# Performance work log

Measured on AMD Instinct MI355X. Metric: run time of the kernel, lower is better.

The kernel has to match this reference:

```python
import jax, jax.numpy as jnp
import numpy as np

NUM_CLASSES = 80
NUM_TOP_QUERIES = 300


def setup_inputs() -> dict:
    key = jax.random.key(0)
    k1, k2, k3 = jax.random.split(key, 3)
    B, Q, C = 256, 1000, NUM_CLASSES
    pred_logits = jax.random.normal(k1, (B, Q, C), dtype=jnp.float32)
    pred_boxes = jax.random.uniform(k2, (B, Q, 4), dtype=jnp.float32)  # cxcywh in [0,1)
    orig_target_sizes = jax.random.uniform(k3, (B, 2), dtype=jnp.float32)  # (W, H) scale
    return {"pred_logits": pred_logits, "pred_boxes": pred_boxes,
            "orig_target_sizes": orig_target_sizes}


def _box_cxcywh_to_xyxy(boxes):
    cx, cy, w, h = jnp.split(boxes, 4, axis=-1)
    return jnp.concatenate([cx - 0.5 * w, cy - 0.5 * h, cx + 0.5 * w, cy + 0.5 * h], axis=-1)


def reference(pred_logits, pred_boxes, orig_target_sizes):
    B, Q, C = pred_logits.shape
    # cxcywh -> xyxy, then scale by [W, H, W, H]
    bbox_pred = _box_cxcywh_to_xyxy(pred_boxes)
    scale = jnp.tile(orig_target_sizes, (1, 2))[:, None, :]  # [B,1,4]
    bbox_pred = bbox_pred * scale
    # focal-loss path: sigmoid + flattened top-k over (Q*C)
    scores_all = jax.nn.sigmoid(pred_logits).reshape(B, Q * C)
    scores, index = jax.lax.top_k(scores_all, NUM_TOP_QUERIES)  # [B,K]
    labels = index % C
    q_index = index // C
    boxes = jnp.take_along_axis(bbox_pred, q_index[:, :, None], axis=1)  # [B,K,4]
    return labels, boxes, scores
```

## Files before the change

kernel.cpp:

```cpp
#include <hip/hip_runtime.h>
#include <hip/hip_bf16.h>

#define BATCH 256
#define NQ 1000
#define NC 80
#define QC 80000
#define KTOP 300
#define NT 1024
#define NBINS 4096
#define CAP 1024
#define T0 2.55f

__device__ __forceinline__ unsigned mono_key(float x) {
    unsigned u = __float_as_uint(x);
    return (u & 0x80000000u) ? ~u : (u | 0x80000000u);
}
__device__ __forceinline__ float inv_key(unsigned k) {
    unsigned u = (k & 0x80000000u) ? (k & 0x7FFFFFFFu) : ~k;
    return __uint_as_float(u);
}

__device__ __forceinline__ float ref_sigmoid(float x) {
    float in = __fmul_rn(0.5f, x);
    float xc = fminf(fmaxf(in, -7.90531110763549805f), 7.90531110763549805f);
    float x2 = __fmul_rn(xc, xc);
    float p = fmaf(x2, -2.76076847742355e-16f, 2.00018790482477e-13f);
    p = fmaf(x2, p, -8.60467152213735e-11f);
    p = fmaf(x2, p,  5.12229709037114e-08f);
    p = fmaf(x2, p,  1.48572235717979e-05f);
    p = fmaf(x2, p,  6.37261928875436e-04f);
    p = fmaf(x2, p,  4.89352455891786e-03f);
    float num = __fmul_rn(xc, p);
    float den = fmaf(x2, 1.19825839466702e-06f, 1.18534705686654e-04f);
    den = fmaf(x2, den, 2.26843463243900e-03f);
    den = fmaf(x2, den, 4.89352518554385e-03f);
    float t = num / den;
    t = (fabsf(in) < 0.0004f) ? in : t;
    return __fadd_rn(0.5f, __fmul_rn(0.5f, t));
}

__global__ __launch_bounds__(NT)
void rtdetr_post_kernel(const float* __restrict__ logits,
                        const float* __restrict__ boxes,
                        const float* __restrict__ sizes,
                        float* __restrict__ out) {
    __shared__ unsigned long long cand[CAP];
    __shared__ unsigned hist[NBINS];
    __shared__ unsigned scan[NT];
    __shared__ unsigned s_tbin, s_count;

    const int b = blockIdx.x;
    const int tid = threadIdx.x;
    const float4* lg4 = (const float4*)(logits + (size_t)b * QC);

    if (tid == 0) s_count = 0;
    __syncthreads();

    for (int i = tid; i < QC / 4; i += NT) {
        float4 v = lg4[i];
        float xs[4] = {v.x, v.y, v.z, v.w};
        #pragma unroll
        for (int j = 0; j < 4; ++j) {
            if (xs[j] >= T0) {
                unsigned pos = atomicAdd(&s_count, 1u);
                if (pos < CAP) {
                    unsigned sk = mono_key(ref_sigmoid(xs[j]));
                    unsigned idx = (unsigned)(i * 4 + j);
                    cand[pos] = ((unsigned long long)sk << 32) | (unsigned)(~idx);
                }
            }
        }
    }
    __syncthreads();
    unsigned cnt = s_count;

    if (cnt < KTOP || cnt > CAP) {
        for (int i = tid; i < NBINS; i += NT) hist[i] = 0;
        if (tid == 0) s_count = 0;
        __syncthreads();
        for (int i = tid; i < QC / 4; i += NT) {
            float4 v = lg4[i];
            atomicAdd(&hist[mono_key(v.x) >> 20], 1u);
            atomicAdd(&hist[mono_key(v.y) >> 20], 1u);
            atomicAdd(&hist[mono_key(v.z) >> 20], 1u);
            atomicAdd(&hist[mono_key(v.w) >> 20], 1u);
        }
        __syncthreads();
        unsigned h0 = hist[tid * 4 + 0], h1 = hist[tid * 4 + 1];
        unsigned h2 = hist[tid * 4 + 2], h3 = hist[tid * 4 + 3];
        scan[tid] = h0 + h1 + h2 + h3;
        __syncthreads();
        for (int off = 1; off < NT; off <<= 1) {
            unsigned v = (tid + off < NT) ? scan[tid + off] : 0u;
            __syncthreads();
            scan[tid] += v;
            __syncthreads();
        }
        unsigned run = (tid + 1 < NT) ? scan[tid + 1] : 0u;
        unsigned hs[4] = {h3, h2, h1, h0};
        #pragma unroll
        for (int j = 0; j < 4; ++j) {
            unsigned bin = (unsigned)(tid * 4 + (3 - j));
            if (run < KTOP && KTOP <= run + hs[j]) s_tbin = bin;
            run += hs[j];
        }
        __syncthreads();
        unsigned thresh = s_tbin << 20;
        thresh = (thresh >= 4096u) ? thresh - 4096u : 0u;
        for (int i = tid; i < QC / 4; i += NT) {
            float4 v = lg4[i];
            float xs[4] = {v.x, v.y, v.z, v.w};
            #pragma unroll
            for (int j = 0; j < 4; ++j) {
                if (mono_key(xs[j]) >= thresh) {
                    unsigned pos = atomicAdd(&s_count, 1u);
                    if (pos < CAP) {
                        unsigned sk = mono_key(ref_sigmoid(xs[j]));
                        unsigned idx = (unsigned)(i * 4 + j);
                        cand[pos] = ((unsigned long long)sk << 32) | (unsigned)(~idx);
                    }
                }
            }
        }
        __syncthreads();
        cnt = s_count; if (cnt > CAP) cnt = CAP;
    }

    if (tid < (int)cnt) {
        unsigned long long my = cand[tid];
        unsigned rank = 0;
        for (unsigned j = 0; j < cnt; ++j) rank += (cand[j] > my) ? 1u : 0u;
        if (rank < KTOP) {
            unsigned sk = (unsigned)(my >> 32);
            unsigned idx = ~((unsigned)my);
            float score = inv_key(sk);
            unsigned label = idx % NC;
            unsigned qi = idx / NC;
            float4 bx = ((const float4*)boxes)[(size_t)b * NQ + qi];
            float W = sizes[b * 2 + 0];
            float H = sizes[b * 2 + 1];
            float x0 = (bx.x - 0.5f * bx.z) * W;
            float y0 = (bx.y - 0.5f * bx.w) * H;
            float x1 = (bx.x + 0.5f * bx.z) * W;
            float y1 = (bx.y + 0.5f * bx.w) * H;
            int o = b * KTOP + (int)rank;
            out[o] = (float)label;
            float* ob = out + BATCH * KTOP;
            ob[(size_t)o * 4 + 0] = x0;
            ob[(size_t)o * 4 + 1] = y0;
            ob[(size_t)o * 4 + 2] = x1;
            ob[(size_t)o * 4 + 3] = y1;
            float* os = out + BATCH * KTOP * 5;
            os[o] = score;
        }
    }
}

extern "C" void kernel_launch(void* const* d_in, const int* in_sizes, int n_in,
                              void* d_out, int out_size, void* d_ws, size_t ws_size,
                              hipStream_t stream) {
    const float* logits = (const float*)d_in[0];
    const float* boxes  = (const float*)d_in[1];
    const float* sizes  = (const float*)d_in[2];
    float* out = (float*)d_out;
    rtdetr_post_kernel<<<BATCH, NT, 0, stream>>>(logits, boxes, sizes, out);
}
```

Baseline: 128.7 us.

## Split threshold scan across multiple blocks per batch with global candidate buffer

Moves the first pass, which filters logits above a fixed threshold, into its own kernel that launches 8 blocks of 256 threads per batch row instead of one 1024-thread block per row. This spreads the memory-bound read over many more workgroups. Candidates are appended to a workspace buffer through global atomics, and a second kernel copies them into shared memory to rank and write the output, running the histogram fallback when needed. The cost is a memset, an extra kernel launch, global atomic contention, and a round trip of the candidate keys through global memory.

```diff
diff --git a/kernel.cpp b/kernel.cpp
--- a/kernel.cpp
+++ b/kernel.cpp
@@ -6,10 +6,14 @@
 #define NC 80
 #define QC 80000
 #define KTOP 300
-#define NT 1024
 #define NBINS 4096
 #define CAP 1024
 #define T0 2.55f
+
+#define SLICES 8
+#define K1_NT 256
+#define F4_PER_SLICE (QC / 4 / SLICES)
+#define K2_NT 1024
 
 __device__ __forceinline__ unsigned mono_key(float x) {
     unsigned u = __float_as_uint(x);
@@ -39,46 +43,59 @@
     return __fadd_rn(0.5f, __fmul_rn(0.5f, t));
 }
 
-__global__ __launch_bounds__(NT)
-void rtdetr_post_kernel(const float* __restrict__ logits,
-                        const float* __restrict__ boxes,
-                        const float* __restrict__ sizes,
-                        float* __restrict__ out) {
-    __shared__ unsigned long long cand[CAP];
-    __shared__ unsigned hist[NBINS];
-    __shared__ unsigned scan[NT];
-    __shared__ unsigned s_tbin, s_count;
+__global__ __launch_bounds__(K1_NT)
+void scan_kernel(const float* __restrict__ logits,
+                 unsigned* __restrict__ counters,
+                 unsigned long long* __restrict__ ckeys) {
+    const int blk = blockIdx.x;
+    const int b = blk / SLICES;
+    const int s = blk % SLICES;
+    const float4* lg4 = (const float4*)(logits + (size_t)b * QC) + s * F4_PER_SLICE;
+    const int base4 = s * F4_PER_SLICE;
 
-    const int b = blockIdx.x;
-    const int tid = threadIdx.x;
-    const float4* lg4 = (const float4*)(logits + (size_t)b * QC);
-
-    if (tid == 0) s_count = 0;
-    __syncthreads();
-
-    for (int i = tid; i < QC / 4; i += NT) {
+    for (int i = threadIdx.x; i < F4_PER_SLICE; i += K1_NT) {
         float4 v = lg4[i];
         float xs[4] = {v.x, v.y, v.z, v.w};
         #pragma unroll
         for (int j = 0; j < 4; ++j) {
             if (xs[j] >= T0) {
-                unsigned pos = atomicAdd(&s_count, 1u);
+                unsigned pos = atomicAdd(&counters[b], 1u);
                 if (pos < CAP) {
                     unsigned sk = mono_key(ref_sigmoid(xs[j]));
-                    unsigned idx = (unsigned)(i * 4 + j);
-                    cand[pos] = ((unsigned long long)sk << 32) | (unsigned)(~idx);
+                    unsigned idx = (unsigned)((base4 + i) * 4 + j);
+                    ckeys[(size_t)b * CAP + pos] =
+                        ((unsigned long long)sk << 32) | (unsigned)(~idx);
                 }
             }
         }
     }
-    __syncthreads();
-    unsigned cnt = s_count;
+}
 
-    if (cnt < KTOP || cnt > CAP) {
-        for (int i = tid; i < NBINS; i += NT) hist[i] = 0;
+__global__ __launch_bounds__(K2_NT)
+void select_kernel(const float* __restrict__ logits,
+                   const float* __restrict__ boxes,
+                   const float* __restrict__ sizes,
+                   const unsigned* __restrict__ counters,
+                   const unsigned long long* __restrict__ ckeys,
+                   float* __restrict__ out) {
+    __shared__ unsigned long long cand[CAP];
+    __shared__ unsigned hist[NBINS];
+    __shared__ unsigned scan[K2_NT];
+    __shared__ unsigned s_tbin, s_count;
+
+    const int b = blockIdx.x;
+    const int tid = threadIdx.x;
+    unsigned cnt = counters[b];
+
+    if (cnt >= KTOP && cnt <= CAP) {
+        if (tid < (int)cnt) cand[tid] = ckeys[(size_t)b * CAP + tid];
+        __syncthreads();
+    } else {
+        const float4* lg4 = (const float4*)(logits + (size_t)b * QC);
+        for (int i = tid; i < NBINS; i += K2_NT) hist[i] = 0;
         if (tid == 0) s_count = 0;
         __syncthreads();
-        for (int i = tid; i < QC / 4; i += NT) {
+        for (int i = tid; i < QC / 4; i += K2_NT) {
             float4 v = lg4[i];
             atomicAdd(&hist[mono_key(v.x) >> 20], 1u);
             atomicAdd(&hist[mono_key(v.y) >> 20], 1u);
@@ -90,13 +107,13 @@
         unsigned h2 = hist[tid * 4 + 2], h3 = hist[tid * 4 + 3];
         scan[tid] = h0 + h1 + h2 + h3;
         __syncthreads();
-        for (int off = 1; off < NT; off <<= 1) {
-            unsigned v = (tid + off < NT) ? scan[tid + off] : 0u;
+        for (int off = 1; off < K2_NT; off <<= 1) {
+            unsigned v = (tid + off < K2_NT) ? scan[tid + off] : 0u;
             __syncthreads();
             scan[tid] += v;
             __syncthreads();
         }
-        unsigned run = (tid + 1 < NT) ? scan[tid + 1] : 0u;
+        unsigned run = (tid + 1 < K2_NT) ? scan[tid + 1] : 0u;
         unsigned hs[4] = {h3, h2, h1, h0};
         #pragma unroll
         for (int j = 0; j < 4; ++j) {
@@ -107,7 +124,7 @@
         __syncthreads();
         unsigned thresh = s_tbin << 20;
         thresh = (thresh >= 4096u) ? thresh - 4096u : 0u;
-        for (int i = tid; i < QC / 4; i += NT) {
+        for (int i = tid; i < QC / 4; i += K2_NT) {
             float4 v = lg4[i];
             float xs[4] = {v.x, v.y, v.z, v.w};
             #pragma unroll
@@ -163,5 +180,11 @@
     const float* boxes  = (const float*)d_in[1];
     const float* sizes  = (const float*)d_in[2];
     float* out = (float*)d_out;
-    rtdetr_post_kernel<<<BATCH, NT, 0, stream>>>(logits, boxes, sizes, out);
+
+    unsigned* counters = (unsigned*)d_ws;
+    unsigned long long* ckeys = (unsigned long long*)((char*)d_ws + 1024);
+
+    hipMemsetAsync(counters, 0, BATCH * sizeof(unsigned), stream);
+    scan_kernel<<<BATCH * SLICES, K1_NT, 0, stream>>>(logits, counters, ckeys);
+    select_kernel<<<BATCH, K2_NT, 0, stream>>>(logits, boxes, sizes, counters, ckeys, out);
 }
```

Result: slower. 224.6 us (+74.5%).
